# Kernel optimization log

Measured on AMD Instinct MI355X. Metric: run time of the kernel, lower is better.

The kernel has to match this reference:

```python
import jax, jax.numpy as jnp
import numpy as np

B, T, C, H = 16, 1024, 768, 64

def setup_inputs() -> dict:
    key = jax.random.key(0)
    ks = jax.random.split(key, 4)
    s = 1.0 / np.sqrt(C)
    return {
        "x": jax.random.normal(ks[0], (B, T, C), dtype=jnp.float32),
        "Wq": jax.random.normal(ks[1], (C, H), dtype=jnp.float32) * s,
        "bq": jnp.zeros((H,), dtype=jnp.float32),
        "Wk": jax.random.normal(ks[2], (C, H), dtype=jnp.float32) * s,
        "bk": jnp.zeros((H,), dtype=jnp.float32),
        "Wv": jax.random.normal(ks[3], (C, H), dtype=jnp.float32) * s,
        "bv": jnp.zeros((H,), dtype=jnp.float32),
    }

def reference(x, Wq, bq, Wk, bk, Wv, bv):
    # single-head causal attention (dropout = eval/identity)
    q = x @ Wq + bq          # [B,T,H]
    k = x @ Wk + bk          # [B,T,H]
    v = x @ Wv + bv          # [B,T,H]
    scale = 1.0 / jnp.sqrt(jnp.asarray(q.shape[-1], q.dtype))
    wei = jnp.einsum("bth,bsh->bts", q, k) * scale  # [B,T,T]
    causal = jnp.tril(jnp.ones((q.shape[1], q.shape[1]), dtype=bool))
    wei = jnp.where(causal, wei, -jnp.inf)
    wei = jax.nn.softmax(wei, axis=-1)
    out = jnp.einsum("bts,bsh->bth", wei, v)        # [B,T,H]
    return out
```

## Files before the change

kernel.cpp:

```cpp
#include <hip/hip_runtime.h>
#include <hip/hip_bf16.h>
#include <math.h>

#define B_ 16
#define T_ 1024
#define C_ 768
#define H_ 64

typedef __attribute__((ext_vector_type(8))) short bf16x8;
typedef __attribute__((ext_vector_type(4))) float f32x4;

__device__ __forceinline__ short f2bf(float f) {
  union { float f; unsigned u; } un;
  un.f = f;
  unsigned r = un.u + 0x7FFFu + ((un.u >> 16) & 1u);
  return (short)(r >> 16);
}

__global__ __launch_bounds__(256) void prep_w(
    const float* __restrict__ Wq, const float* __restrict__ Wk,
    const float* __restrict__ Wv, short* __restrict__ wfrag) {
  const int o = blockIdx.x * 256 + threadIdx.x;
  const int j = o & 7;
  const int l = (o >> 3) & 63;
  const int fid = o >> 9;
  const int ct = fid % 12;
  const int ks = fid / 12;
  const int mat = ct >> 2;
  const int col = (ct & 3) * 16 + (l & 15);
  const int k = ks * 32 + (l >> 4) * 8 + j;
  const float* W = (mat == 0) ? Wq : (mat == 1) ? Wk : Wv;
  wfrag[o] = f2bf(W[(size_t)k * H_ + col]);
}

#define QKV_LDSF 6400

__global__ __launch_bounds__(128, 2) void qkv_gemm(
    const float* __restrict__ x, const short* __restrict__ wfrag,
    const float* __restrict__ bq, const float* __restrict__ bk,
    const float* __restrict__ bv, short* __restrict__ qkv) {
  __shared__ float lds[QKV_LDSF];
  const int rt = blockIdx.x;
  const int w  = threadIdx.x >> 6;
  const int l  = threadIdx.x & 63;
  const int lo = l & 15, hi = l >> 4;
  const int kh = w;

  float* stg = lds + w * 3072;
  const char* xb = (const char*)(x + (size_t)rt * 16 * C_ + kh * 384);

  auto STAGE = [&](int buf, int c) {
    #pragma unroll
    for (int s = 0; s < 4; ++s) {
      const int r = s * 4 + hi;
      const char* src = xb + (size_t)r * (C_ * 4) + (size_t)c * 256
                        + ((lo * 16) ^ ((r & 7) << 4));
      float* dst = stg + buf * 1024 + s * 256;
      __builtin_amdgcn_global_load_lds(
          (const __attribute__((address_space(1))) void*)src,
          (__attribute__((address_space(3))) void*)dst, 16, 0, 0);
    }
  };

  f32x4 acc[12];
  #pragma unroll
  for (int ct = 0; ct < 12; ++ct) acc[ct] = (f32x4){0.f, 0.f, 0.f, 0.f};

  STAGE(0, 0);
  STAGE(1, 1);

  #pragma unroll
  for (int c = 0; c < 6; ++c) {
    const int buf = c % 3;
    __builtin_amdgcn_sched_barrier(0);
    bf16x8 wf0[12], wf1[12];
    const int ksb = kh * 12 + c * 2;
    #pragma unroll
    for (int ct = 0; ct < 12; ++ct) {
      wf0[ct] = *(const bf16x8*)(wfrag + ((size_t)(ksb * 12 + ct) << 9) + l * 8);
      wf1[ct] = *(const bf16x8*)(wfrag + ((size_t)((ksb + 1) * 12 + ct) << 9) + l * 8);
    }
    __builtin_amdgcn_sched_barrier(0);
    if (c < 4) STAGE((c + 2) % 3, c + 2);
    __builtin_amdgcn_sched_barrier(0);
    if (c < 4)      { asm volatile("s_waitcnt vmcnt(32)" ::: "memory"); }
    else if (c < 5) { asm volatile("s_waitcnt vmcnt(28)" ::: "memory"); }
    else            { asm volatile("s_waitcnt vmcnt(24)" ::: "memory"); }
    __builtin_amdgcn_sched_barrier(0);
    bf16x8 af0, af1;
    {
      const char* rp = (const char*)(stg + buf * 1024) + lo * 256;
      const int sw = (lo & 7) << 4;
      f32x4 x0 = *(const f32x4*)(rp + ((hi * 32)       ^ sw));
      f32x4 x1 = *(const f32x4*)(rp + ((hi * 32 + 16)  ^ sw));
      f32x4 x2 = *(const f32x4*)(rp + ((128 + hi * 32)      ^ sw));
      f32x4 x3 = *(const f32x4*)(rp + ((128 + hi * 32 + 16) ^ sw));
      #pragma unroll
      for (int j = 0; j < 4; ++j) {
        af0[j] = f2bf(x0[j]); af0[4 + j] = f2bf(x1[j]);
        af1[j] = f2bf(x2[j]); af1[4 + j] = f2bf(x3[j]);
      }
    }
    __builtin_amdgcn_s_setprio(1);
    #pragma unroll
    for (int ct = 0; ct < 12; ++ct)
      acc[ct] = __builtin_amdgcn_mfma_f32_16x16x32_bf16(af0, wf0[ct], acc[ct], 0, 0, 0);
    #pragma unroll
    for (int ct = 0; ct < 12; ++ct)
      acc[ct] = __builtin_amdgcn_mfma_f32_16x16x32_bf16(af1, wf1[ct], acc[ct], 0, 0, 0);
    __builtin_amdgcn_s_setprio(0);
  }

  __syncthreads();
  #pragma unroll
  for (int ct = 0; ct < 12; ++ct)
    #pragma unroll
    for (int r = 0; r < 4; ++r)
      lds[w * 3136 + (hi * 4 + r) * 196 + ct * 16 + lo] = acc[ct][r];
  __syncthreads();

  {
    const int row = threadIdx.x >> 3;
    const int c0 = (threadIdx.x & 7) * 24;
    bf16x8 o0, o1, o2;
    #pragma unroll
    for (int j = 0; j < 24; ++j) {
      const int col = c0 + j;
      float s = lds[row * 196 + col] + lds[3136 + row * 196 + col];
      const int mat = col >> 6;
      const float* bb = (mat == 0) ? bq : (mat == 1) ? bk : bv;
      s += bb[col & 63];
      const short v = f2bf(s);
      if (j < 8) o0[j] = v; else if (j < 16) o1[j - 8] = v; else o2[j - 16] = v;
    }
    short* op = qkv + ((size_t)(rt * 16 + row)) * 192 + c0;
    *(bf16x8*)(op)      = o0;
    *(bf16x8*)(op + 8)  = o1;
    *(bf16x8*)(op + 16) = o2;
  }
}

__global__ __launch_bounds__(256) void vtrans(const short* __restrict__ qkv,
                                              short* __restrict__ vt) {
  __shared__ short tile[64][66];
  const int b = blockIdx.y;
  const int tb = blockIdx.x * 64;
  const int tid = threadIdx.x;

  {
    const int tt = tid >> 2, c = (tid & 3) * 16;
    const short* src = qkv + (size_t)(b * T_ + tb + tt) * 192 + 128 + c;
    bf16x8 v0 = *(const bf16x8*)(src);
    bf16x8 v1 = *(const bf16x8*)(src + 8);
    #pragma unroll
    for (int j = 0; j < 8; ++j) { tile[tt][c + j] = v0[j]; tile[tt][c + 8 + j] = v1[j]; }
  }
  __syncthreads();
  {
    const int n = tid >> 2, toff = (tid & 3) * 16;
    short* dst = vt + ((size_t)(b * H_ + n)) * T_ + tb + toff;
    bf16x8 o0, o1;
    #pragma unroll
    for (int j = 0; j < 8; ++j) { o0[j] = tile[toff + j][n]; o1[j] = tile[toff + 8 + j][n]; }
    *(bf16x8*)(dst) = o0;
    *(bf16x8*)(dst + 8) = o1;
  }
}

#define SCALE_LOG2E 0.18033688011114382f

__global__ __launch_bounds__(256) void flash(
    const short* __restrict__ qkv, const short* __restrict__ vt,
    float* __restrict__ out) {
  __shared__ __align__(16) short p_lds[4][2][16][72];
  __shared__ float o_sh[4][16][64];
  __shared__ float ml_sh[4][2][2][16];

  const int wgid = blockIdx.x;
  const int kk = wgid >> 3;
  const int qp = 31 - (kk & 31);
  const int b  = (wgid & 7) + 8 * (kk >> 5);

  const int w = threadIdx.x >> 6;
  const int l = threadIdx.x & 63;
  const int lo = l & 15, hi = l >> 4;
  const int off = hi * 4;

  const int qt0 = 2 * qp, qt1 = 2 * qp + 1;
  const int dtile = qt0 >> 2;
  const int ntot = dtile + 1;
  const int span = (ntot + 3) >> 2;
  const int kv0 = w * span;
  const int kv1 = min(ntot, kv0 + span);
  const int qr0 = qt0 & 3, qr1 = qr0 + 1;

  const short* qrowA = qkv + (size_t)(b * T_ + qt0 * 16 + lo) * 192;
  bf16x8 qA0 = *(const bf16x8*)(qrowA + hi * 8);
  bf16x8 qA1 = *(const bf16x8*)(qrowA + 32 + hi * 8);
  const short* qrowB = qkv + (size_t)(b * T_ + qt1 * 16 + lo) * 192;
  bf16x8 qB0 = *(const bf16x8*)(qrowB + hi * 8);
  bf16x8 qB1 = *(const bf16x8*)(qrowB + 32 + hi * 8);

  float mA = -1e30f, lsA = 0.f;
  float mB = -1e30f, lsB = 0.f;
  f32x4 oA[4], oB[4];
  #pragma unroll
  for (int dt = 0; dt < 4; ++dt) {
    oA[dt] = (f32x4){0.f, 0.f, 0.f, 0.f};
    oB[dt] = (f32x4){0.f, 0.f, 0.f, 0.f};
  }

  for (int kvt = kv0; kvt < kv1; ++kvt) {
    const bool diag = (kvt == dtile);
    const int nctA = diag ? (qr0 + 1) : 4;
    const int nctB = diag ? (qr1 + 1) : 4;

    bf16x8 kf[8], vf[8];
    #pragma unroll
    for (int ct = 0; ct < 4; ++ct) {
      const short* krow = qkv + (size_t)(b * T_ + kvt * 64 + ct * 16 + lo) * 192 + 64;
      kf[2 * ct]     = *(const bf16x8*)(krow + hi * 8);
      kf[2 * ct + 1] = *(const bf16x8*)(krow + 32 + hi * 8);
    }
    #pragma unroll
    for (int dt = 0; dt < 4; ++dt) {
      const short* vrow = vt + (size_t)(b * H_ + dt * 16 + lo) * T_ + kvt * 64;
      vf[2 * dt]     = *(const bf16x8*)(vrow + hi * 8);
      vf[2 * dt + 1] = *(const bf16x8*)(vrow + 32 + hi * 8);
    }

    f32x4 svA[4], svB[4];
    #pragma unroll
    for (int ct = 0; ct < 4; ++ct) {
      svA[ct] = (f32x4){0.f, 0.f, 0.f, 0.f};
      svB[ct] = (f32x4){0.f, 0.f, 0.f, 0.f};
    }
    __builtin_amdgcn_s_setprio(1);
    #pragma unroll
    for (int ct = 0; ct < 4; ++ct) {
      if (ct < nctA) {
        svA[ct] = __builtin_amdgcn_mfma_f32_16x16x32_bf16(kf[2 * ct], qA0, svA[ct], 0, 0, 0);
        svA[ct] = __builtin_amdgcn_mfma_f32_16x16x32_bf16(kf[2 * ct + 1], qA1, svA[ct], 0, 0, 0);
      }
      if (ct < nctB) {
        svB[ct] = __builtin_amdgcn_mfma_f32_16x16x32_bf16(kf[2 * ct], qB0, svB[ct], 0, 0, 0);
        svB[ct] = __builtin_amdgcn_mfma_f32_16x16x32_bf16(kf[2 * ct + 1], qB1, svB[ct], 0, 0, 0);
      }
    }
    __builtin_amdgcn_s_setprio(0);

    #pragma unroll
    for (int ct = 0; ct < 4; ++ct) {
      #pragma unroll
      for (int r = 0; r < 4; ++r) {
        float sA = (ct < nctA) ? svA[ct][r] * SCALE_LOG2E : -1e30f;
        if (diag && ct == qr0 && (off + r) > lo) sA = -1e30f;
        svA[ct][r] = sA;
        float sB = (ct < nctB) ? svB[ct][r] * SCALE_LOG2E : -1e30f;
        if (diag && ct == qr1 && (off + r) > lo) sB = -1e30f;
        svB[ct][r] = sB;
      }
    }

    {
      float tmax = svA[0][0];
      #pragma unroll
      for (int ct = 0; ct < 4; ++ct)
        #pragma unroll
        for (int r = 0; r < 4; ++r) tmax = fmaxf(tmax, svA[ct][r]);
      tmax = fmaxf(tmax, __shfl_xor(tmax, 16));
      tmax = fmaxf(tmax, __shfl_xor(tmax, 32));
      if (!__all(tmax - mA <= 8.0f)) {
        const float mn = fmaxf(mA, tmax);
        const float corr = exp2f(mA - mn);
        mA = mn;
        lsA *= corr;
        #pragma unroll
        for (int r = 0; r < 4; ++r) {
          const float cr = __shfl(corr, off + r);
          #pragma unroll
          for (int dt = 0; dt < 4; ++dt) oA[dt][r] *= cr;
        }
      }
      float psum = 0.f;
      #pragma unroll
      for (int ct = 0; ct < 4; ++ct) {
        #pragma unroll
        for (int r = 0; r < 4; ++r) {
          float p = exp2f(svA[ct][r] - mA);
          svA[ct][r] = p;
          psum += p;
        }
      }
      psum += __shfl_xor(psum, 16);
      psum += __shfl_xor(psum, 32);
      lsA += psum;
      #pragma unroll
      for (int ct = 0; ct < 4; ++ct) {
        __hip_bfloat162 p01 = __float22bfloat162_rn(float2{svA[ct][0], svA[ct][1]});
        __hip_bfloat162 p23 = __float22bfloat162_rn(float2{svA[ct][2], svA[ct][3]});
        uint2 pk;
        pk.x = *reinterpret_cast<unsigned*>(&p01);
        pk.y = *reinterpret_cast<unsigned*>(&p23);
        *reinterpret_cast<uint2*>(&p_lds[w][0][lo][ct * 16 + off]) = pk;
      }
    }
    {
      float tmax = svB[0][0];
      #pragma unroll
      for (int ct = 0; ct < 4; ++ct)
        #pragma unroll
        for (int r = 0; r < 4; ++r) tmax = fmaxf(tmax, svB[ct][r]);
      tmax = fmaxf(tmax, __shfl_xor(tmax, 16));
      tmax = fmaxf(tmax, __shfl_xor(tmax, 32));
      if (!__all(tmax - mB <= 8.0f)) {
        const float mn = fmaxf(mB, tmax);
        const float corr = exp2f(mB - mn);
        mB = mn;
        lsB *= corr;
        #pragma unroll
        for (int r = 0; r < 4; ++r) {
          const float cr = __shfl(corr, off + r);
          #pragma unroll
          for (int dt = 0; dt < 4; ++dt) oB[dt][r] *= cr;
        }
      }
      float psum = 0.f;
      #pragma unroll
      for (int ct = 0; ct < 4; ++ct) {
        #pragma unroll
        for (int r = 0; r < 4; ++r) {
          float p = exp2f(svB[ct][r] - mB);
          svB[ct][r] = p;
          psum += p;
        }
      }
      psum += __shfl_xor(psum, 16);
      psum += __shfl_xor(psum, 32);
      lsB += psum;
      #pragma unroll
      for (int ct = 0; ct < 4; ++ct) {
        __hip_bfloat162 p01 = __float22bfloat162_rn(float2{svB[ct][0], svB[ct][1]});
        __hip_bfloat162 p23 = __float22bfloat162_rn(float2{svB[ct][2], svB[ct][3]});
        uint2 pk;
        pk.x = *reinterpret_cast<unsigned*>(&p01);
        pk.y = *reinterpret_cast<unsigned*>(&p23);
        *reinterpret_cast<uint2*>(&p_lds[w][1][lo][ct * 16 + off]) = pk;
      }
    }

    bf16x8 paA0 = *(const bf16x8*)(&p_lds[w][0][lo][hi * 8]);
    bf16x8 paA1 = *(const bf16x8*)(&p_lds[w][0][lo][32 + hi * 8]);
    bf16x8 paB0 = *(const bf16x8*)(&p_lds[w][1][lo][hi * 8]);
    bf16x8 paB1 = *(const bf16x8*)(&p_lds[w][1][lo][32 + hi * 8]);
    __builtin_amdgcn_s_setprio(1);
    #pragma unroll
    for (int dt = 0; dt < 4; ++dt) {
      oA[dt] = __builtin_amdgcn_mfma_f32_16x16x32_bf16(paA0, vf[2 * dt], oA[dt], 0, 0, 0);
      oA[dt] = __builtin_amdgcn_mfma_f32_16x16x32_bf16(paA1, vf[2 * dt + 1], oA[dt], 0, 0, 0);
      oB[dt] = __builtin_amdgcn_mfma_f32_16x16x32_bf16(paB0, vf[2 * dt], oB[dt], 0, 0, 0);
      oB[dt] = __builtin_amdgcn_mfma_f32_16x16x32_bf16(paB1, vf[2 * dt + 1], oB[dt], 0, 0, 0);
    }
    __builtin_amdgcn_s_setprio(0);
  }

  if (hi == 0) {
    ml_sh[w][0][0][lo] = mA;  ml_sh[w][0][1][lo] = lsA;
    ml_sh[w][1][0][lo] = mB;  ml_sh[w][1][1][lo] = lsB;
  }

  #pragma unroll
  for (int dt = 0; dt < 4; ++dt)
    #pragma unroll
    for (int r = 0; r < 4; ++r)
      o_sh[w][off + r][dt * 16 + lo] = oA[dt][r];
  __syncthreads();
  {
    const int row = threadIdx.x >> 4;
    const int c0 = (threadIdx.x & 15) * 4;
    float M = fmaxf(fmaxf(ml_sh[0][0][0][row], ml_sh[1][0][0][row]),
                    fmaxf(ml_sh[2][0][0][row], ml_sh[3][0][0][row]));
    float e[4];
    float L = 0.f;
    #pragma unroll
    for (int w2 = 0; w2 < 4; ++w2) {
      e[w2] = exp2f(ml_sh[w2][0][0][row] - M);
      L += ml_sh[w2][0][1][row] * e[w2];
    }
    f32x4 o;
    #pragma unroll
    for (int j = 0; j < 4; ++j) {
      float O = 0.f;
      #pragma unroll
      for (int w2 = 0; w2 < 4; ++w2) O += e[w2] * o_sh[w2][row][c0 + j];
      o[j] = O / L;
    }
    *(f32x4*)(out + (size_t)(b * T_ + qt0 * 16 + row) * H_ + c0) = o;
  }
  __syncthreads();
  #pragma unroll
  for (int dt = 0; dt < 4; ++dt)
    #pragma unroll
    for (int r = 0; r < 4; ++r)
      o_sh[w][off + r][dt * 16 + lo] = oB[dt][r];
  __syncthreads();
  {
    const int row = threadIdx.x >> 4;
    const int c0 = (threadIdx.x & 15) * 4;
    float M = fmaxf(fmaxf(ml_sh[0][1][0][row], ml_sh[1][1][0][row]),
                    fmaxf(ml_sh[2][1][0][row], ml_sh[3][1][0][row]));
    float e[4];
    float L = 0.f;
    #pragma unroll
    for (int w2 = 0; w2 < 4; ++w2) {
      e[w2] = exp2f(ml_sh[w2][1][0][row] - M);
      L += ml_sh[w2][1][1][row] * e[w2];
    }
    f32x4 o;
    #pragma unroll
    for (int j = 0; j < 4; ++j) {
      float O = 0.f;
      #pragma unroll
      for (int w2 = 0; w2 < 4; ++w2) O += e[w2] * o_sh[w2][row][c0 + j];
      o[j] = O / L;
    }
    *(f32x4*)(out + (size_t)(b * T_ + qt1 * 16 + row) * H_ + c0) = o;
  }
}

extern "C" void kernel_launch(void* const* d_in, const int* in_sizes, int n_in,
                              void* d_out, int out_size, void* d_ws, size_t ws_size,
                              hipStream_t stream) {
  const float* x  = (const float*)d_in[0];
  const float* Wq = (const float*)d_in[1];
  const float* bq = (const float*)d_in[2];
  const float* Wk = (const float*)d_in[3];
  const float* bk = (const float*)d_in[4];
  const float* Wv = (const float*)d_in[5];
  const float* bv = (const float*)d_in[6];
  float* out = (float*)d_out;

  short* wfrag = (short*)d_ws;
  short* qkv = wfrag + (size_t)3 * H_ * C_;
  short* vtb = qkv + (size_t)B_ * T_ * 192;

  prep_w<<<dim3(576), dim3(256), 0, stream>>>(Wq, Wk, Wv, wfrag);
  qkv_gemm<<<dim3(1024), dim3(128), 0, stream>>>(x, wfrag, bq, bk, bv, qkv);
  vtrans<<<dim3(T_ / 64, B_), dim3(256), 0, stream>>>(qkv, vtb);
  flash<<<dim3(512), dim3(256), 0, stream>>>(qkv, vtb, out);
}
```

Baseline: 51.85 us.

## Restructure QKV GEMM to 32-row tiles with 32x32 MFMA and 4-way K split

The QKV projection GEMM now processes 32 rows per block with 4 waves, each wave covering a quarter of the K dimension. It uses 32x32x16 bf16 MFMAs in place of 16x16x32, and the weight fragment layout in prep_w is changed to match. Staging goes from triple to double buffering, and the four partial sums are reduced through LDS in two steps. The aim is to reuse each weight fragment load across more rows and to issue fewer, larger MFMAs. The cost is more LDS traffic in the reduction, extra syncs, and half as many blocks.

```diff
diff --git a/kernel.cpp b/kernel.cpp
--- a/kernel.cpp
+++ b/kernel.cpp
@@ -9,6 +9,7 @@
 
 typedef __attribute__((ext_vector_type(8))) short bf16x8;
 typedef __attribute__((ext_vector_type(4))) float f32x4;
+typedef __attribute__((ext_vector_type(16))) float f32x16;
 
 __device__ __forceinline__ short f2bf(float f) {
   union { float f; unsigned u; } un;
@@ -23,117 +24,129 @@
   const int o = blockIdx.x * 256 + threadIdx.x;
   const int j = o & 7;
   const int l = (o >> 3) & 63;
-  const int fid = o >> 9;
-  const int ct = fid % 12;
-  const int ks = fid / 12;
-  const int mat = ct >> 2;
-  const int col = (ct & 3) * 16 + (l & 15);
-  const int k = ks * 32 + (l >> 4) * 8 + j;
+  const int f = o >> 9;
+  const int ct = f % 6;
+  const int ks = f / 6;
+  const int col = ct * 32 + (l & 31);
+  const int mat = col >> 6;
+  const int ncol = col & 63;
+  const int k = ks * 16 + (l >> 5) * 8 + j;
   const float* W = (mat == 0) ? Wq : (mat == 1) ? Wk : Wv;
-  wfrag[o] = f2bf(W[(size_t)k * H_ + col]);
-}
-
-#define QKV_LDSF 6400
-
-__global__ __launch_bounds__(128, 2) void qkv_gemm(
+  wfrag[o] = f2bf(W[(size_t)k * H_ + ncol]);
+}
+
+#define QKV_LDSF 16384
+
+__global__ __launch_bounds__(256, 2) void qkv_gemm(
     const float* __restrict__ x, const short* __restrict__ wfrag,
     const float* __restrict__ bq, const float* __restrict__ bk,
     const float* __restrict__ bv, short* __restrict__ qkv) {
   __shared__ float lds[QKV_LDSF];
   const int rt = blockIdx.x;
-  const int w  = threadIdx.x >> 6;
-  const int l  = threadIdx.x & 63;
-  const int lo = l & 15, hi = l >> 4;
-  const int kh = w;
-
-  float* stg = lds + w * 3072;
-  const char* xb = (const char*)(x + (size_t)rt * 16 * C_ + kh * 384);
+  const int tid = threadIdx.x;
+  const int w  = tid >> 6;
+  const int l  = tid & 63;
+  const int lo5 = l & 31;
+  const int hi1 = l >> 5;
+
+  float* stg = lds + w * 4096;
+  const char* xb = (const char*)(x + (size_t)rt * 32 * C_ + w * 192);
 
   auto STAGE = [&](int buf, int c) {
     #pragma unroll
-    for (int s = 0; s < 4; ++s) {
-      const int r = s * 4 + hi;
-      const char* src = xb + (size_t)r * (C_ * 4) + (size_t)c * 256
-                        + ((lo * 16) ^ ((r & 7) << 4));
-      float* dst = stg + buf * 1024 + s * 256;
+    for (int s = 0; s < 8; ++s) {
+      const int row = s * 4 + (l >> 4);
+      const char* src = xb + (size_t)row * (C_ * 4) + (size_t)c * 256
+                        + (((l & 15) ^ (row & 15)) << 4);
+      float* dst = stg + buf * 2048 + s * 256;
       __builtin_amdgcn_global_load_lds(
           (const __attribute__((address_space(1))) void*)src,
           (__attribute__((address_space(3))) void*)dst, 16, 0, 0);
     }
   };
 
-  f32x4 acc[12];
+  f32x16 acc[6];
   #pragma unroll
-  for (int ct = 0; ct < 12; ++ct) acc[ct] = (f32x4){0.f, 0.f, 0.f, 0.f};
+  for (int ct = 0; ct < 6; ++ct)
+    #pragma unroll
+    for (int r = 0; r < 16; ++r) acc[ct][r] = 0.f;
 
   STAGE(0, 0);
-  STAGE(1, 1);
 
   #pragma unroll
-  for (int c = 0; c < 6; ++c) {
-    const int buf = c % 3;
+  for (int c = 0; c < 3; ++c) {
+    const int buf = c & 1;
     __builtin_amdgcn_sched_barrier(0);
-    bf16x8 wf0[12], wf1[12];
-    const int ksb = kh * 12 + c * 2;
-    #pragma unroll
-    for (int ct = 0; ct < 12; ++ct) {
-      wf0[ct] = *(const bf16x8*)(wfrag + ((size_t)(ksb * 12 + ct) << 9) + l * 8);
-      wf1[ct] = *(const bf16x8*)(wfrag + ((size_t)((ksb + 1) * 12 + ct) << 9) + l * 8);
-    }
+    bf16x8 wf[4][6];
+    #pragma unroll
+    for (int t = 0; t < 4; ++t)
+      #pragma unroll
+      for (int ct = 0; ct < 6; ++ct)
+        wf[t][ct] = *(const bf16x8*)(wfrag
+            + ((size_t)((w * 12 + c * 4 + t) * 6 + ct) << 9) + l * 8);
     __builtin_amdgcn_sched_barrier(0);
-    if (c < 4) STAGE((c + 2) % 3, c + 2);
+    if (c < 2) STAGE(buf ^ 1, c + 1);
     __builtin_amdgcn_sched_barrier(0);
-    if (c < 4)      { asm volatile("s_waitcnt vmcnt(32)" ::: "memory"); }
-    else if (c < 5) { asm volatile("s_waitcnt vmcnt(28)" ::: "memory"); }
-    else            { asm volatile("s_waitcnt vmcnt(24)" ::: "memory"); }
+    if (c < 2) { asm volatile("s_waitcnt vmcnt(32)" ::: "memory"); }
+    else       { asm volatile("s_waitcnt vmcnt(24)" ::: "memory"); }
     __builtin_amdgcn_sched_barrier(0);
-    bf16x8 af0, af1;
-    {
-      const char* rp = (const char*)(stg + buf * 1024) + lo * 256;
-      const int sw = (lo & 7) << 4;
-      f32x4 x0 = *(const f32x4*)(rp + ((hi * 32)       ^ sw));
-      f32x4 x1 = *(const f32x4*)(rp + ((hi * 32 + 16)  ^ sw));
-      f32x4 x2 = *(const f32x4*)(rp + ((128 + hi * 32)      ^ sw));
-      f32x4 x3 = *(const f32x4*)(rp + ((128 + hi * 32 + 16) ^ sw));
-      #pragma unroll
-      for (int j = 0; j < 4; ++j) {
-        af0[j] = f2bf(x0[j]); af0[4 + j] = f2bf(x1[j]);
-        af1[j] = f2bf(x2[j]); af1[4 + j] = f2bf(x3[j]);
-      }
-    }
-    __builtin_amdgcn_s_setprio(1);
-    #pragma unroll
-    for (int ct = 0; ct < 12; ++ct)
-      acc[ct] = __builtin_amdgcn_mfma_f32_16x16x32_bf16(af0, wf0[ct], acc[ct], 0, 0, 0);
-    #pragma unroll
-    for (int ct = 0; ct < 12; ++ct)
-      acc[ct] = __builtin_amdgcn_mfma_f32_16x16x32_bf16(af1, wf1[ct], acc[ct], 0, 0, 0);
-    __builtin_amdgcn_s_setprio(0);
-  }
-
-  __syncthreads();
-  #pragma unroll
-  for (int ct = 0; ct < 12; ++ct)
-    #pragma unroll
-    for (int r = 0; r < 4; ++r)
-      lds[w * 3136 + (hi * 4 + r) * 196 + ct * 16 + lo] = acc[ct][r];
+    #pragma unroll
+    for (int t = 0; t < 4; ++t) {
+      const char* rb = (const char*)(stg + buf * 2048) + lo5 * 256;
+      const int m = lo5 & 15;
+      const int g0 = t * 4 + hi1 * 2;
+      f32x4 x0 = *(const f32x4*)(rb + (((g0)     ^ m) << 4));
+      f32x4 x1 = *(const f32x4*)(rb + (((g0 + 1) ^ m) << 4));
+      bf16x8 af;
+      #pragma unroll
+      for (int j = 0; j < 4; ++j) { af[j] = f2bf(x0[j]); af[4 + j] = f2bf(x1[j]); }
+      __builtin_amdgcn_s_setprio(1);
+      #pragma unroll
+      for (int ct = 0; ct < 6; ++ct)
+        acc[ct] = __builtin_amdgcn_mfma_f32_32x32x16_bf16(af, wf[t][ct], acc[ct], 0, 0, 0);
+      __builtin_amdgcn_s_setprio(0);
+    }
+  }
+
+  __syncthreads();
+  float* pool = lds;
+  if (w < 2) {
+    #pragma unroll
+    for (int ct = 0; ct < 6; ++ct)
+      #pragma unroll
+      for (int r = 0; r < 16; ++r) {
+        const int row = (r & 3) + 8 * (r >> 2) + 4 * hi1;
+        pool[w * 6400 + row * 200 + ct * 32 + lo5] = acc[ct][r];
+      }
+  }
+  __syncthreads();
+  if (w >= 2) {
+    #pragma unroll
+    for (int ct = 0; ct < 6; ++ct)
+      #pragma unroll
+      for (int r = 0; r < 16; ++r) {
+        const int row = (r & 3) + 8 * (r >> 2) + 4 * hi1;
+        float* p = &pool[(w - 2) * 6400 + row * 200 + ct * 32 + lo5];
+        *p += acc[ct][r];
+      }
+  }
   __syncthreads();
 
   {
-    const int row = threadIdx.x >> 3;
-    const int c0 = (threadIdx.x & 7) * 24;
+    const int row = tid >> 3;
+    const int c0 = (tid & 7) * 24;
     bf16x8 o0, o1, o2;
     #pragma unroll
     for (int j = 0; j < 24; ++j) {
       const int col = c0 + j;
-      float s = lds[row * 196 + col] + lds[3136 + row * 196 + col];
+      float s = pool[row * 200 + col] + pool[6400 + row * 200 + col];
       const int mat = col >> 6;
       const float* bb = (mat == 0) ? bq : (mat == 1) ? bk : bv;
       s += bb[col & 63];
       const short v = f2bf(s);
       if (j < 8) o0[j] = v; else if (j < 16) o1[j - 8] = v; else o2[j - 16] = v;
     }
-    short* op = qkv + ((size_t)(rt * 16 + row)) * 192 + c0;
+    short* op = qkv + ((size_t)(rt * 32 + row)) * 192 + c0;
     *(bf16x8*)(op)      = o0;
     *(bf16x8*)(op + 8)  = o1;
     *(bf16x8*)(op + 16) = o2;
@@ -445,7 +458,7 @@
   short* vtb = qkv + (size_t)B_ * T_ * 192;
 
   prep_w<<<dim3(576), dim3(256), 0, stream>>>(Wq, Wk, Wv, wfrag);
-  qkv_gemm<<<dim3(1024), dim3(128), 0, stream>>>(x, wfrag, bq, bk, bv, qkv);
+  qkv_gemm<<<dim3(512), dim3(256), 0, stream>>>(x, wfrag, bq, bk, bv, qkv);
   vtrans<<<dim3(T_ / 64, B_), dim3(256), 0, stream>>>(qkv, vtb);
   flash<<<dim3(512), dim3(256), 0, stream>>>(qkv, vtb, out);
 }
```

Result: faster. 50.49 us (-2.6%).

## Fuse V transpose into QKV GEMM epilogue and split K across four waves

Applied to the files above, without the earlier changes.

The QKV projection kernel now runs with four waves per block, each covering a quarter of the 768-wide reduction, and reduces the partial sums through LDS. Its epilogue writes Q and K into a compact 128-wide buffer and writes V directly in transposed layout, so the separate vtrans kernel and its extra global round-trip go away. The staging pipeline is reduced to double buffering, and the weight fragment loads are split into two halves to lower register pressure. The trade-offs are extra LDS reduction traffic and synchronization, plus transposed V stores that are only 8 bytes wide.

```diff
diff --git a/kernel.cpp b/kernel.cpp
--- a/kernel.cpp
+++ b/kernel.cpp
@@ -8,6 +8,7 @@
 #define H_ 64
 
 typedef __attribute__((ext_vector_type(8))) short bf16x8;
+typedef __attribute__((ext_vector_type(4))) short bf16x4;
 typedef __attribute__((ext_vector_type(4))) float f32x4;
 
 __device__ __forceinline__ short f2bf(float f) {
@@ -33,21 +34,22 @@
   wfrag[o] = f2bf(W[(size_t)k * H_ + col]);
 }
 
-#define QKV_LDSF 6400
-
-__global__ __launch_bounds__(128, 2) void qkv_gemm(
+#define QKV_LDSF 8192
+
+__global__ __launch_bounds__(256, 3) void qkv_gemm(
     const float* __restrict__ x, const short* __restrict__ wfrag,
     const float* __restrict__ bq, const float* __restrict__ bk,
-    const float* __restrict__ bv, short* __restrict__ qkv) {
+    const float* __restrict__ bv,
+    short* __restrict__ qk, short* __restrict__ vt) {
   __shared__ float lds[QKV_LDSF];
   const int rt = blockIdx.x;
-  const int w  = threadIdx.x >> 6;
-  const int l  = threadIdx.x & 63;
+  const int tid = threadIdx.x;
+  const int w  = tid >> 6;
+  const int l  = tid & 63;
   const int lo = l & 15, hi = l >> 4;
-  const int kh = w;
-
-  float* stg = lds + w * 3072;
-  const char* xb = (const char*)(x + (size_t)rt * 16 * C_ + kh * 384);
+
+  float* stg = lds + w * 2048;
+  const char* xb = (const char*)(x + (size_t)rt * 16 * C_ + w * 192);
 
   auto STAGE = [&](int buf, int c) {
     #pragma unroll
@@ -70,22 +72,17 @@
   STAGE(1, 1);
 
   #pragma unroll
-  for (int c = 0; c < 6; ++c) {
-    const int buf = c % 3;
+  for (int c = 0; c < 3; ++c) {
+    const int buf = c & 1;
+    const int ksb = w * 6 + c * 2;
     __builtin_amdgcn_sched_barrier(0);
-    bf16x8 wf0[12], wf1[12];
-    const int ksb = kh * 12 + c * 2;
-    #pragma unroll
-    for (int ct = 0; ct < 12; ++ct) {
+    bf16x8 wf0[12];
+    #pragma unroll
+    for (int ct = 0; ct < 12; ++ct)
       wf0[ct] = *(const bf16x8*)(wfrag + ((size_t)(ksb * 12 + ct) << 9) + l * 8);
-      wf1[ct] = *(const bf16x8*)(wfrag + ((size_t)((ksb + 1) * 12 + ct) << 9) + l * 8);
-    }
     __builtin_amdgcn_sched_barrier(0);
-    if (c < 4) STAGE((c + 2) % 3, c + 2);
-    __builtin_amdgcn_sched_barrier(0);
-    if (c < 4)      { asm volatile("s_waitcnt vmcnt(32)" ::: "memory"); }
-    else if (c < 5) { asm volatile("s_waitcnt vmcnt(28)" ::: "memory"); }
-    else            { asm volatile("s_waitcnt vmcnt(24)" ::: "memory"); }
+    if (c < 2) { asm volatile("s_waitcnt vmcnt(16)" ::: "memory"); }
+    else       { asm volatile("s_waitcnt vmcnt(12)" ::: "memory"); }
     __builtin_amdgcn_sched_barrier(0);
     bf16x8 af0, af1;
     {
@@ -105,72 +102,79 @@
     #pragma unroll
     for (int ct = 0; ct < 12; ++ct)
       acc[ct] = __builtin_amdgcn_mfma_f32_16x16x32_bf16(af0, wf0[ct], acc[ct], 0, 0, 0);
+    __builtin_amdgcn_s_setprio(0);
+    __builtin_amdgcn_sched_barrier(0);
+    bf16x8 wf1[12];
+    #pragma unroll
+    for (int ct = 0; ct < 12; ++ct)
+      wf1[ct] = *(const bf16x8*)(wfrag + ((size_t)((ksb + 1) * 12 + ct) << 9) + l * 8);
+    __builtin_amdgcn_sched_barrier(0);
+    __builtin_amdgcn_s_setprio(1);
     #pragma unroll
     for (int ct = 0; ct < 12; ++ct)
       acc[ct] = __builtin_amdgcn_mfma_f32_16x16x32_bf16(af1, wf1[ct], acc[ct], 0, 0, 0);
     __builtin_amdgcn_s_setprio(0);
-  }
-
-  __syncthreads();
-  #pragma unroll
-  for (int ct = 0; ct < 12; ++ct)
-    #pragma unroll
-    for (int r = 0; r < 4; ++r)
-      lds[w * 3136 + (hi * 4 + r) * 196 + ct * 16 + lo] = acc[ct][r];
+    if (c == 0) {
+      __builtin_amdgcn_sched_barrier(0);
+      STAGE(0, 2);
+    }
+  }
+
+  __syncthreads();
+  float* pool = lds;
+  if (w < 2) {
+    #pragma unroll
+    for (int ct = 0; ct < 12; ++ct)
+      #pragma unroll
+      for (int r = 0; r < 4; ++r)
+        pool[w * 3200 + (hi * 4 + r) * 200 + ct * 16 + lo] = acc[ct][r];
+  }
+  __syncthreads();
+  if (w >= 2) {
+    #pragma unroll
+    for (int ct = 0; ct < 12; ++ct)
+      #pragma unroll
+      for (int r = 0; r < 4; ++r) {
+        float* p = &pool[(w - 2) * 3200 + (hi * 4 + r) * 200 + ct * 16 + lo];
+        *p += acc[ct][r];
+      }
+  }
   __syncthreads();
 
   {
-    const int row = threadIdx.x >> 3;
-    const int c0 = (threadIdx.x & 7) * 24;
-    bf16x8 o0, o1, o2;
-    #pragma unroll
-    for (int j = 0; j < 24; ++j) {
+    const int row = tid >> 4;
+    const int c0 = (tid & 15) * 8;
+    bf16x8 o;
+    #pragma unroll
+    for (int j = 0; j < 8; ++j) {
       const int col = c0 + j;
-      float s = lds[row * 196 + col] + lds[3136 + row * 196 + col];
-      const int mat = col >> 6;
-      const float* bb = (mat == 0) ? bq : (mat == 1) ? bk : bv;
-      s += bb[col & 63];
-      const short v = f2bf(s);
-      if (j < 8) o0[j] = v; else if (j < 16) o1[j - 8] = v; else o2[j - 16] = v;
-    }
-    short* op = qkv + ((size_t)(rt * 16 + row)) * 192 + c0;
-    *(bf16x8*)(op)      = o0;
-    *(bf16x8*)(op + 8)  = o1;
-    *(bf16x8*)(op + 16) = o2;
+      float s = pool[row * 200 + col] + pool[3200 + row * 200 + col];
+      s += (col < 64) ? bq[col] : bk[col - 64];
+      o[j] = f2bf(s);
+    }
+    *(bf16x8*)(qk + ((size_t)(rt * 16 + row)) * 128 + c0) = o;
+  }
+  {
+    const int n = tid >> 2;
+    const int sub = tid & 3;
+    const int b = rt >> 6;
+    const int tloc = (rt & 63) * 16;
+    const float bias_v = bv[n];
+    bf16x4 o;
+    #pragma unroll
+    for (int j = 0; j < 4; ++j) {
+      const int row = sub * 4 + j;
+      float s = pool[row * 200 + 128 + n] + pool[3200 + row * 200 + 128 + n];
+      o[j] = f2bf(s + bias_v);
+    }
+    *(bf16x4*)(vt + ((size_t)(b * H_ + n)) * T_ + tloc + sub * 4) = o;
   }
 }
 
-__global__ __launch_bounds__(256) void vtrans(const short* __restrict__ qkv,
-                                              short* __restrict__ vt) {
-  __shared__ short tile[64][66];
-  const int b = blockIdx.y;
-  const int tb = blockIdx.x * 64;
-  const int tid = threadIdx.x;
-
-  {
-    const int tt = tid >> 2, c = (tid & 3) * 16;
-    const short* src = qkv + (size_t)(b * T_ + tb + tt) * 192 + 128 + c;
-    bf16x8 v0 = *(const bf16x8*)(src);
-    bf16x8 v1 = *(const bf16x8*)(src + 8);
-    #pragma unroll
-    for (int j = 0; j < 8; ++j) { tile[tt][c + j] = v0[j]; tile[tt][c + 8 + j] = v1[j]; }
-  }
-  __syncthreads();
-  {
-    const int n = tid >> 2, toff = (tid & 3) * 16;
-    short* dst = vt + ((size_t)(b * H_ + n)) * T_ + tb + toff;
-    bf16x8 o0, o1;
-    #pragma unroll
-    for (int j = 0; j < 8; ++j) { o0[j] = tile[toff + j][n]; o1[j] = tile[toff + 8 + j][n]; }
-    *(bf16x8*)(dst) = o0;
-    *(bf16x8*)(dst + 8) = o1;
-  }
-}
-
 #define SCALE_LOG2E 0.18033688011114382f
 
 __global__ __launch_bounds__(256) void flash(
-    const short* __restrict__ qkv, const short* __restrict__ vt,
+    const short* __restrict__ qk, const short* __restrict__ vt,
     float* __restrict__ out) {
   __shared__ __align__(16) short p_lds[4][2][16][72];
   __shared__ float o_sh[4][16][64];
@@ -194,10 +198,10 @@
   const int kv1 = min(ntot, kv0 + span);
   const int qr0 = qt0 & 3, qr1 = qr0 + 1;
 
-  const short* qrowA = qkv + (size_t)(b * T_ + qt0 * 16 + lo) * 192;
+  const short* qrowA = qk + (size_t)(b * T_ + qt0 * 16 + lo) * 128;
   bf16x8 qA0 = *(const bf16x8*)(qrowA + hi * 8);
   bf16x8 qA1 = *(const bf16x8*)(qrowA + 32 + hi * 8);
-  const short* qrowB = qkv + (size_t)(b * T_ + qt1 * 16 + lo) * 192;
+  const short* qrowB = qk + (size_t)(b * T_ + qt1 * 16 + lo) * 128;
   bf16x8 qB0 = *(const bf16x8*)(qrowB + hi * 8);
   bf16x8 qB1 = *(const bf16x8*)(qrowB + 32 + hi * 8);
 
@@ -218,7 +222,7 @@
     bf16x8 kf[8], vf[8];
     #pragma unroll
     for (int ct = 0; ct < 4; ++ct) {
-      const short* krow = qkv + (size_t)(b * T_ + kvt * 64 + ct * 16 + lo) * 192 + 64;
+      const short* krow = qk + (size_t)(b * T_ + kvt * 64 + ct * 16 + lo) * 128 + 64;
       kf[2 * ct]     = *(const bf16x8*)(krow + hi * 8);
       kf[2 * ct + 1] = *(const bf16x8*)(krow + 32 + hi * 8);
     }
@@ -441,11 +445,10 @@
   float* out = (float*)d_out;
 
   short* wfrag = (short*)d_ws;
-  short* qkv = wfrag + (size_t)3 * H_ * C_;
-  short* vtb = qkv + (size_t)B_ * T_ * 192;
+  short* qk = wfrag + (size_t)3 * H_ * C_;
+  short* vtb = qk + (size_t)B_ * T_ * 128;
 
   prep_w<<<dim3(576), dim3(256), 0, stream>>>(Wq, Wk, Wv, wfrag);
-  qkv_gemm<<<dim3(1024), dim3(128), 0, stream>>>(x, wfrag, bq, bk, bv, qkv);
-  vtrans<<<dim3(T_ / 64, B_), dim3(256), 0, stream>>>(qkv, vtb);
-  flash<<<dim3(512), dim3(256), 0, stream>>>(qkv, vtb, out);
+  qkv_gemm<<<dim3(1024), dim3(256), 0, stream>>>(x, wfrag, bq, bk, bv, qk, vtb);
+  flash<<<dim3(512), dim3(256), 0, stream>>>(qk, vtb, out);
 }
```

Measured after the change: 48.39 us. 6.7% less time.
